# Kernel optimization log

Hardware: AMD Instinct MI355X
Metric: run time of the kernel (lower is better)

The kernel has to match this reference:

```python
import jax, jax.numpy as jnp
import numpy as np

BN_EPS = 1e-3  # Keras BatchNormalization default epsilon

def _conv2d_same(x, w, b):
    # x: NHWC, w: HWIO (kh,kw,2,1)
    y = jax.lax.conv_general_dilated(x, w, window_strides=(1, 1), padding='SAME',
                                     dimension_numbers=('NHWC', 'HWIO', 'NHWC'))
    return y + b

def _zpool(t):
    # concat([max, avg], axis=-1) over channel axis -> last dim = 2
    return jnp.concatenate([jnp.max(t, axis=-1, keepdims=True),
                            jnp.mean(t, axis=-1, keepdims=True)], axis=-1)

def _att_map(t2, w, b, g, beta, mean, var):
    y = _conv2d_same(t2, w, b)
    y = (y - mean) * jax.lax.rsqrt(var + BN_EPS) * g + beta  # inference BN
    return jax.nn.sigmoid(y)

def setup_inputs() -> dict:
    key = jax.random.key(0)
    ks = jax.random.split(key, 8)
    B, H, W, C, K, RR = 32, 56, 56, 256, 7, 8
    d = {}
    d['x'] = jax.random.normal(ks[0], (B, H, W, C), dtype=jnp.float32)
    for i, kk in zip((1, 2, 3), ks[1:4]):
        d[f'conv{i}_w'] = jax.random.normal(kk, (K, K, 2, 1), dtype=jnp.float32) * 0.1
        d[f'conv{i}_b'] = jnp.zeros((1,), dtype=jnp.float32)
        d[f'bn{i}_g'] = jnp.ones((1,), dtype=jnp.float32)
        d[f'bn{i}_b'] = jnp.zeros((1,), dtype=jnp.float32)
        d[f'bn{i}_m'] = jnp.zeros((1,), dtype=jnp.float32)
        d[f'bn{i}_v'] = jnp.ones((1,), dtype=jnp.float32)
    Ch = C // RR
    d['se_w1'] = jax.random.normal(ks[4], (C, Ch), dtype=jnp.float32) * (2.0 / C) ** 0.5
    d['se_b1'] = jnp.zeros((Ch,), dtype=jnp.float32)
    d['se_w2'] = jax.random.normal(ks[5], (Ch, C), dtype=jnp.float32) * 0.05
    d['se_b2'] = jnp.zeros((C,), dtype=jnp.float32)
    return d

def reference(x, conv1_w, conv1_b, bn1_g, bn1_b, bn1_m, bn1_v,
              conv2_w, conv2_b, bn2_g, bn2_b, bn2_m, bn2_v,
              conv3_w, conv3_b, bn3_g, bn3_b, bn3_m, bn3_v,
              se_w1, se_b1, se_w2, se_b2):
    # Branch 1 (H-axis): permute (B,H,W,C)->(B,H,C,W), pool over W
    th1 = jnp.transpose(x, (0, 1, 3, 2))
    a1 = _att_map(_zpool(th1), conv1_w, conv1_b, bn1_g, bn1_b, bn1_m, bn1_v)
    br1 = jnp.transpose(th1 * a1, (0, 1, 3, 2))
    # Branch 2 (W-axis): permute (B,H,W,C)->(B,C,W,H), pool over H
    th2 = jnp.transpose(x, (0, 3, 2, 1))
    a2 = _att_map(_zpool(th2), conv2_w, conv2_b, bn2_g, bn2_b, bn2_m, bn2_v)
    br2 = jnp.transpose(th2 * a2, (0, 3, 2, 1))
    # Branch 3 (identity): pool over C
    a3 = _att_map(_zpool(x), conv3_w, conv3_b, bn3_g, bn3_b, bn3_m, bn3_v)
    br3 = x * a3
    # TriSE1: Add branches, then SE channel gating
    s = br1 + br2 + br3
    gap = jnp.mean(s, axis=(1, 2), keepdims=True)            # (B,1,1,C)
    h = jax.nn.relu(jnp.einsum('bijc,cd->bijd', gap, se_w1) + se_b1)
    cw = jax.nn.sigmoid(jnp.einsum('bijd,dc->bijc', h, se_w2) + se_b2)
    return s * cw
```

## Files before the change

kernel.cpp:

```cpp
#include <hip/hip_runtime.h>
#include <math.h>

namespace {
constexpr int B = 32, H = 56, W = 56, C = 256;
constexpr int HW  = H * W;
constexpr int WC  = W * C;
constexpr int HC  = H * C;
constexpr int HWC = H * W * C;
constexpr int CH  = 32;
constexpr float BN_EPS = 1e-3f;

__device__ __forceinline__ float sigmoidf_(float v) { return 1.0f / (1.0f + expf(-v)); }
}

__global__ __launch_bounds__(256)
void pool_all_kernel(const float* __restrict__ x,
                     float* __restrict__ pmax1, float* __restrict__ pavg1,
                     float* __restrict__ pmax2, float* __restrict__ pavg2,
                     float* __restrict__ pmax3, float* __restrict__ pavg3) {
    const int t = threadIdx.x;
    const int lane = t & 63, sub = t >> 6;
    const int c4 = lane * 4;
    __shared__ float smx[4][256];
    __shared__ float ssm[4][256];

    if (blockIdx.x < B * H) {
        const int b = blockIdx.x / H, h = blockIdx.x % H;
        const float* xp = x + (size_t)b * HWC + (size_t)h * WC;
        float4 mx = make_float4(-INFINITY, -INFINITY, -INFINITY, -INFINITY);
        float4 sm = make_float4(0.f, 0.f, 0.f, 0.f);
        for (int wq = 0; wq < 14; ++wq) {
            const int w = wq * 4 + sub;
            const float4 v = *(const float4*)(xp + w * C + c4);
            mx.x = fmaxf(mx.x, v.x); mx.y = fmaxf(mx.y, v.y);
            mx.z = fmaxf(mx.z, v.z); mx.w = fmaxf(mx.w, v.w);
            sm.x += v.x; sm.y += v.y; sm.z += v.z; sm.w += v.w;
            float m3 = fmaxf(fmaxf(v.x, v.y), fmaxf(v.z, v.w));
            float s3 = v.x + v.y + v.z + v.w;
            #pragma unroll
            for (int off = 32; off > 0; off >>= 1) {
                m3 = fmaxf(m3, __shfl_down(m3, off));
                s3 += __shfl_down(s3, off);
            }
            if (lane == 0) {
                pmax3[b * HW + h * W + w] = m3;
                pavg3[b * HW + h * W + w] = s3 * (1.0f / C);
            }
        }
        *(float4*)&smx[sub][c4] = mx;
        *(float4*)&ssm[sub][c4] = sm;
        __syncthreads();
        const float m = fmaxf(fmaxf(smx[0][t], smx[1][t]), fmaxf(smx[2][t], smx[3][t]));
        const float s = ssm[0][t] + ssm[1][t] + ssm[2][t] + ssm[3][t];
        pmax1[b * HC + h * C + t] = m;
        pavg1[b * HC + h * C + t] = s * (1.0f / W);
    } else {
        const int tt = blockIdx.x - B * H;
        const int b = tt / W, w = tt % W;
        const float* xp = x + (size_t)b * HWC + (size_t)w * C;
        float4 mx = make_float4(-INFINITY, -INFINITY, -INFINITY, -INFINITY);
        float4 sm = make_float4(0.f, 0.f, 0.f, 0.f);
        for (int hq = 0; hq < 14; ++hq) {
            const int h = hq * 4 + sub;
            const float4 v = *(const float4*)(xp + (size_t)h * WC + c4);
            mx.x = fmaxf(mx.x, v.x); mx.y = fmaxf(mx.y, v.y);
            mx.z = fmaxf(mx.z, v.z); mx.w = fmaxf(mx.w, v.w);
            sm.x += v.x; sm.y += v.y; sm.z += v.z; sm.w += v.w;
        }
        *(float4*)&smx[sub][c4] = mx;
        *(float4*)&ssm[sub][c4] = sm;
        __syncthreads();
        const float m = fmaxf(fmaxf(smx[0][t], smx[1][t]), fmaxf(smx[2][t], smx[3][t]));
        const float s = ssm[0][t] + ssm[1][t] + ssm[2][t] + ssm[3][t];
        pmax2[b * WC + w * C + t] = m;
        pavg2[b * WC + w * C + t] = s * (1.0f / H);
    }
}

__global__ __launch_bounds__(256)
void conv_all_kernel(const float* __restrict__ pmax1, const float* __restrict__ pavg1,
                     const float* __restrict__ pmax2, const float* __restrict__ pavg2,
                     const float* __restrict__ pmax3, const float* __restrict__ pavg3,
                     const float* __restrict__ c1w, const float* __restrict__ c1b,
                     const float* __restrict__ g1,  const float* __restrict__ be1,
                     const float* __restrict__ m1,  const float* __restrict__ v1,
                     const float* __restrict__ c2w, const float* __restrict__ c2b,
                     const float* __restrict__ g2,  const float* __restrict__ be2,
                     const float* __restrict__ m2,  const float* __restrict__ v2,
                     const float* __restrict__ c3w, const float* __restrict__ c3b,
                     const float* __restrict__ g3,  const float* __restrict__ be3,
                     const float* __restrict__ m3,  const float* __restrict__ v3,
                     float* __restrict__ a1, float* __restrict__ a2t, float* __restrict__ a3) {
    const int t = threadIdx.x;
    __shared__ float wg[98];

    if (blockIdx.x < B * H) {
        if (t < 98) wg[t] = c1w[t];
        __syncthreads();
        const int b = blockIdx.x / H, h = blockIdx.x % H;
        const float A  = rsqrtf(v1[0] + BN_EPS) * g1[0];
        const float Bc = (c1b[0] - m1[0]) * A + be1[0];
        float acc = 0.f;
        const float* bm = pmax1 + b * HC;
        const float* ba = pavg1 + b * HC;
        #pragma unroll
        for (int ky = 0; ky < 7; ++ky) {
            const int hy = h + ky - 3;
            if (hy < 0 || hy >= H) continue;
            const float* rm = bm + hy * C;
            const float* ra = ba + hy * C;
            #pragma unroll
            for (int kx = 0; kx < 7; ++kx) {
                const int cx = t + kx - 3;
                if (cx < 0 || cx >= C) continue;
                acc += rm[cx] * wg[ky * 14 + kx * 2] + ra[cx] * wg[ky * 14 + kx * 2 + 1];
            }
        }
        a1[b * HC + h * C + t] = sigmoidf_(acc * A + Bc);
    } else if (blockIdx.x < 2 * B * H) {
        if (t < 98) wg[t] = c2w[t];
        __syncthreads();
        const int tt = blockIdx.x - B * H;
        const int b = tt / W, w = tt % W;
        const float A  = rsqrtf(v2[0] + BN_EPS) * g2[0];
        const float Bc = (c2b[0] - m2[0]) * A + be2[0];
        float acc = 0.f;
        #pragma unroll
        for (int kx = 0; kx < 7; ++kx) {
            const int wx = w + kx - 3;
            if (wx < 0 || wx >= W) continue;
            const float* rm = pmax2 + b * WC + wx * C;
            const float* ra = pavg2 + b * WC + wx * C;
            #pragma unroll
            for (int ky = 0; ky < 7; ++ky) {
                const int cy = t + ky - 3;
                if (cy < 0 || cy >= C) continue;
                acc += rm[cy] * wg[ky * 14 + kx * 2] + ra[cy] * wg[ky * 14 + kx * 2 + 1];
            }
        }
        a2t[b * WC + w * C + t] = sigmoidf_(acc * A + Bc);
    } else {
        if (t < 98) wg[t] = c3w[t];
        __syncthreads();
        const int gid = (blockIdx.x - 2 * B * H) * 256 + t;
        const int b = gid / HW;
        const int hw = gid % HW;
        const int h = hw / W, w = hw % W;
        const float A  = rsqrtf(v3[0] + BN_EPS) * g3[0];
        const float Bc = (c3b[0] - m3[0]) * A + be3[0];
        float acc = 0.f;
        const float* bm = pmax3 + b * HW;
        const float* ba = pavg3 + b * HW;
        #pragma unroll
        for (int ky = 0; ky < 7; ++ky) {
            const int hy = h + ky - 3;
            if (hy < 0 || hy >= H) continue;
            #pragma unroll
            for (int kx = 0; kx < 7; ++kx) {
                const int wx = w + kx - 3;
                if (wx < 0 || wx >= W) continue;
                acc += bm[hy * W + wx] * wg[ky * 14 + kx * 2] + ba[hy * W + wx] * wg[ky * 14 + kx * 2 + 1];
            }
        }
        a3[b * HW + hw] = sigmoidf_(acc * A + Bc);
    }
}

__global__ __launch_bounds__(256)
void gap_row_kernel(const float* __restrict__ x, const float* __restrict__ a1,
                    const float* __restrict__ a2t, const float* __restrict__ a3,
                    float* __restrict__ gpart) {
    const int b = blockIdx.x / H, h = blockIdx.x % H;
    const int t = threadIdx.x;
    const int lane = t & 63, sub = t >> 6;
    const int c4 = lane * 4;
    const float* xp  = x   + (size_t)b * HWC + (size_t)h * WC;
    const float* a2b = a2t + (size_t)b * WC;
    const float4 a1v = *(const float4*)(a1 + b * HC + h * C + c4);
    float4 acc = make_float4(0.f, 0.f, 0.f, 0.f);
    for (int wq = 0; wq < 14; ++wq) {
        const int w = wq * 4 + sub;
        const float4 xv  = *(const float4*)(xp  + w * C + c4);
        const float4 a2v = *(const float4*)(a2b + w * C + c4);
        const float a3v  = a3[b * HW + h * W + w];
        acc.x += xv.x * (a1v.x + a2v.x + a3v);
        acc.y += xv.y * (a1v.y + a2v.y + a3v);
        acc.z += xv.z * (a1v.z + a2v.z + a3v);
        acc.w += xv.w * (a1v.w + a2v.w + a3v);
    }
    __shared__ float sacc[4][256];
    *(float4*)&sacc[sub][c4] = acc;
    __syncthreads();
    gpart[(size_t)blockIdx.x * C + t] = sacc[0][t] + sacc[1][t] + sacc[2][t] + sacc[3][t];
}

__global__ __launch_bounds__(256)
void se_kernel(const float* __restrict__ gpart,
               const float* __restrict__ w1, const float* __restrict__ b1,
               const float* __restrict__ w2, const float* __restrict__ b2,
               float* __restrict__ cw) {
    const int b = blockIdx.x;
    const int t = threadIdx.x;
    __shared__ float gs[C];
    __shared__ float hs[CH];
    float s = 0.f;
    for (int r = 0; r < H; ++r) s += gpart[(size_t)(b * H + r) * C + t];
    gs[t] = s * (1.0f / (float)HW);
    __syncthreads();
    if (t < CH) {
        float a = b1[t];
        for (int c = 0; c < C; ++c) a += gs[c] * w1[c * CH + t];
        hs[t] = fmaxf(a, 0.f);
    }
    __syncthreads();
    float a = b2[t];
    #pragma unroll
    for (int d = 0; d < CH; ++d) a += hs[d] * w2[d * C + t];
    cw[b * C + t] = sigmoidf_(a);
}

__global__ __launch_bounds__(256)
void out_row_kernel(const float* __restrict__ x, const float* __restrict__ a1,
                    const float* __restrict__ a2t, const float* __restrict__ a3,
                    const float* __restrict__ cw, float* __restrict__ out) {
    const int b = blockIdx.x / H, h = blockIdx.x % H;
    const int t = threadIdx.x;
    const int lane = t & 63, sub = t >> 6;
    const int c4 = lane * 4;
    const float* xp  = x   + (size_t)b * HWC + (size_t)h * WC;
    const float* a2b = a2t + (size_t)b * WC;
    float*       op  = out + (size_t)b * HWC + (size_t)h * WC;
    const float4 a1v = *(const float4*)(a1 + b * HC + h * C + c4);
    const float4 cwv = *(const float4*)(cw + b * C + c4);
    for (int wq = 0; wq < 14; ++wq) {
        const int w = wq * 4 + sub;
        const float4 xv  = *(const float4*)(xp  + w * C + c4);
        const float4 a2v = *(const float4*)(a2b + w * C + c4);
        const float a3v  = a3[b * HW + h * W + w];
        float4 o;
        o.x = xv.x * (a1v.x + a2v.x + a3v) * cwv.x;
        o.y = xv.y * (a1v.y + a2v.y + a3v) * cwv.y;
        o.z = xv.z * (a1v.z + a2v.z + a3v) * cwv.z;
        o.w = xv.w * (a1v.w + a2v.w + a3v) * cwv.w;
        *(float4*)(op + w * C + c4) = o;
    }
}

extern "C" void kernel_launch(void* const* d_in, const int* in_sizes, int n_in,
                              void* d_out, int out_size, void* d_ws, size_t ws_size,
                              hipStream_t stream) {
    const float* x   = (const float*)d_in[0];
    const float* c1w = (const float*)d_in[1];  const float* c1b = (const float*)d_in[2];
    const float* g1  = (const float*)d_in[3];  const float* be1 = (const float*)d_in[4];
    const float* m1  = (const float*)d_in[5];  const float* v1  = (const float*)d_in[6];
    const float* c2w = (const float*)d_in[7];  const float* c2b = (const float*)d_in[8];
    const float* g2  = (const float*)d_in[9];  const float* be2 = (const float*)d_in[10];
    const float* m2  = (const float*)d_in[11]; const float* v2  = (const float*)d_in[12];
    const float* c3w = (const float*)d_in[13]; const float* c3b = (const float*)d_in[14];
    const float* g3  = (const float*)d_in[15]; const float* be3 = (const float*)d_in[16];
    const float* m3  = (const float*)d_in[17]; const float* v3  = (const float*)d_in[18];
    const float* sw1 = (const float*)d_in[19]; const float* sb1 = (const float*)d_in[20];
    const float* sw2 = (const float*)d_in[21]; const float* sb2 = (const float*)d_in[22];

    float* ws = (float*)d_ws;
    float* pmax1 = ws;
    float* pavg1 = pmax1 + (size_t)B * HC;
    float* pmax2 = pavg1 + (size_t)B * HC;
    float* pavg2 = pmax2 + (size_t)B * WC;
    float* pmax3 = pavg2 + (size_t)B * WC;
    float* pavg3 = pmax3 + (size_t)B * HW;
    float* a1    = pavg3 + (size_t)B * HW;
    float* a2t   = a1    + (size_t)B * HC;
    float* a3    = a2t   + (size_t)B * WC;
    float* gpart = a3    + (size_t)B * HW;
    float* cwv   = gpart + (size_t)B * H * C;

    pool_all_kernel<<<B * H + B * W, 256, 0, stream>>>(x, pmax1, pavg1, pmax2, pavg2, pmax3, pavg3);
    conv_all_kernel<<<2 * B * H + (B * HW) / 256, 256, 0, stream>>>(
        pmax1, pavg1, pmax2, pavg2, pmax3, pavg3,
        c1w, c1b, g1, be1, m1, v1,
        c2w, c2b, g2, be2, m2, v2,
        c3w, c3b, g3, be3, m3, v3,
        a1, a2t, a3);
    gap_row_kernel<<<B * H, 256, 0, stream>>>(x, a1, a2t, a3, gpart);
    se_kernel<<<B, 256, 0, stream>>>(gpart, sw1, sb1, sw2, sb2, cwv);
    out_row_kernel<<<B * H, 256, 0, stream>>>(x, a1, a2t, a3, cwv, (float*)d_out);
}
```

Measured before the change: 311.9 us.

## Factor GAP algebraically, stage conv inputs in LDS, restructure W-pool, nontemporal output

The global-average-pool sum for branches 1 and 2 is rewritten as a1·pavg1 and a2·pavg2 summed in the SE kernel, so gap_row only multiplies x by a3. That cuts the a1/a2 reads from the second full pass over x. The conv kernel stages the 7 needed pooled rows into zero-padded shared memory to drop the per-tap bounds checks. The W-axis pooling now gives each thread its own w column across all H rows, removing the LDS reduction and using far fewer blocks. Output stores become nontemporal. The fewer pooling blocks may reduce parallelism, and the SE kernel now does more serial work per batch.

```diff
diff --git a/kernel.cpp b/kernel.cpp
--- a/kernel.cpp
+++ b/kernel.cpp
@@ -10,7 +10,15 @@
 constexpr int CH  = 32;
 constexpr float BN_EPS = 1e-3f;
 
+using f4v = __attribute__((ext_vector_type(4))) float;
+
 __device__ __forceinline__ float sigmoidf_(float v) { return 1.0f / (1.0f + expf(-v)); }
+
+__device__ __forceinline__ void nt_store_float4(float* p, const float4& o) {
+    union { float4 s; f4v v; } u;
+    u.s = o;
+    __builtin_nontemporal_store(u.v, (f4v*)p);
+}
 }
 
 __global__ __launch_bounds__(256)
@@ -19,12 +27,12 @@
                      float* __restrict__ pmax2, float* __restrict__ pavg2,
                      float* __restrict__ pmax3, float* __restrict__ pavg3) {
     const int t = threadIdx.x;
-    const int lane = t & 63, sub = t >> 6;
-    const int c4 = lane * 4;
-    __shared__ float smx[4][256];
-    __shared__ float ssm[4][256];
 
     if (blockIdx.x < B * H) {
+        const int lane = t & 63, sub = t >> 6;
+        const int c4 = lane * 4;
+        __shared__ float smx[4][256];
+        __shared__ float ssm[4][256];
         const int b = blockIdx.x / H, h = blockIdx.x % H;
         const float* xp = x + (size_t)b * HWC + (size_t)h * WC;
         float4 mx = make_float4(-INFINITY, -INFINITY, -INFINITY, -INFINITY);
@@ -56,24 +64,25 @@
         pavg1[b * HC + h * C + t] = s * (1.0f / W);
     } else {
         const int tt = blockIdx.x - B * H;
-        const int b = tt / W, w = tt % W;
-        const float* xp = x + (size_t)b * HWC + (size_t)w * C;
+        const int b = tt / 14, wq = tt % 14;
+        const int w = wq * 4 + (t >> 6);
+        const int c4 = (t & 63) * 4;
+        const float* xp = x + (size_t)b * HWC + (size_t)w * C + c4;
         float4 mx = make_float4(-INFINITY, -INFINITY, -INFINITY, -INFINITY);
         float4 sm = make_float4(0.f, 0.f, 0.f, 0.f);
-        for (int hq = 0; hq < 14; ++hq) {
-            const int h = hq * 4 + sub;
-            const float4 v = *(const float4*)(xp + (size_t)h * WC + c4);
+        #pragma unroll 8
+        for (int h = 0; h < H; ++h) {
+            const float4 v = *(const float4*)(xp + (size_t)h * WC);
             mx.x = fmaxf(mx.x, v.x); mx.y = fmaxf(mx.y, v.y);
             mx.z = fmaxf(mx.z, v.z); mx.w = fmaxf(mx.w, v.w);
             sm.x += v.x; sm.y += v.y; sm.z += v.z; sm.w += v.w;
         }
-        *(float4*)&smx[sub][c4] = mx;
-        *(float4*)&ssm[sub][c4] = sm;
-        __syncthreads();
-        const float m = fmaxf(fmaxf(smx[0][t], smx[1][t]), fmaxf(smx[2][t], smx[3][t]));
-        const float s = ssm[0][t] + ssm[1][t] + ssm[2][t] + ssm[3][t];
-        pmax2[b * WC + w * C + t] = m;
-        pavg2[b * WC + w * C + t] = s * (1.0f / H);
+        const int oi = b * WC + w * C + c4;
+        *(float4*)(pmax2 + oi) = mx;
+        float4 av;
+        av.x = sm.x * (1.0f / H); av.y = sm.y * (1.0f / H);
+        av.z = sm.z * (1.0f / H); av.w = sm.w * (1.0f / H);
+        *(float4*)(pavg2 + oi) = av;
     }
 }
 
@@ -93,51 +102,59 @@
                      float* __restrict__ a1, float* __restrict__ a2t, float* __restrict__ a3) {
     const int t = threadIdx.x;
     __shared__ float wg[98];
+    __shared__ float sm[7][264];
+    __shared__ float sa[7][264];
 
     if (blockIdx.x < B * H) {
         if (t < 98) wg[t] = c1w[t];
+        const int b = blockIdx.x / H, h = blockIdx.x % H;
+        const float* bm = pmax1 + b * HC;
+        const float* ba = pavg1 + b * HC;
+        #pragma unroll
+        for (int ky = 0; ky < 7; ++ky) {
+            const int hy = h + ky - 3;
+            const bool val = (hy >= 0 && hy < H);
+            const int hyc = min(max(hy, 0), H - 1);
+            const float lm = bm[hyc * C + t];
+            const float la = ba[hyc * C + t];
+            sm[ky][t + 3] = val ? lm : 0.f;
+            sa[ky][t + 3] = val ? la : 0.f;
+            if (t < 3) { sm[ky][t] = 0.f; sa[ky][t] = 0.f; sm[ky][261 - t] = 0.f; sa[ky][261 - t] = 0.f; }
+        }
         __syncthreads();
-        const int b = blockIdx.x / H, h = blockIdx.x % H;
         const float A  = rsqrtf(v1[0] + BN_EPS) * g1[0];
         const float Bc = (c1b[0] - m1[0]) * A + be1[0];
         float acc = 0.f;
-        const float* bm = pmax1 + b * HC;
-        const float* ba = pavg1 + b * HC;
-        #pragma unroll
-        for (int ky = 0; ky < 7; ++ky) {
-            const int hy = h + ky - 3;
-            if (hy < 0 || hy >= H) continue;
-            const float* rm = bm + hy * C;
-            const float* ra = ba + hy * C;
+        #pragma unroll
+        for (int ky = 0; ky < 7; ++ky)
             #pragma unroll
-            for (int kx = 0; kx < 7; ++kx) {
-                const int cx = t + kx - 3;
-                if (cx < 0 || cx >= C) continue;
-                acc += rm[cx] * wg[ky * 14 + kx * 2] + ra[cx] * wg[ky * 14 + kx * 2 + 1];
-            }
-        }
+            for (int kx = 0; kx < 7; ++kx)
+                acc += sm[ky][t + kx] * wg[ky * 14 + kx * 2] + sa[ky][t + kx] * wg[ky * 14 + kx * 2 + 1];
         a1[b * HC + h * C + t] = sigmoidf_(acc * A + Bc);
     } else if (blockIdx.x < 2 * B * H) {
         if (t < 98) wg[t] = c2w[t];
-        __syncthreads();
         const int tt = blockIdx.x - B * H;
         const int b = tt / W, w = tt % W;
+        #pragma unroll
+        for (int kx = 0; kx < 7; ++kx) {
+            const int wx = w + kx - 3;
+            const bool val = (wx >= 0 && wx < W);
+            const int wxc = min(max(wx, 0), W - 1);
+            const float lm = pmax2[b * WC + wxc * C + t];
+            const float la = pavg2[b * WC + wxc * C + t];
+            sm[kx][t + 3] = val ? lm : 0.f;
+            sa[kx][t + 3] = val ? la : 0.f;
+            if (t < 3) { sm[kx][t] = 0.f; sa[kx][t] = 0.f; sm[kx][261 - t] = 0.f; sa[kx][261 - t] = 0.f; }
+        }
+        __syncthreads();
         const float A  = rsqrtf(v2[0] + BN_EPS) * g2[0];
         const float Bc = (c2b[0] - m2[0]) * A + be2[0];
         float acc = 0.f;
         #pragma unroll
-        for (int kx = 0; kx < 7; ++kx) {
-            const int wx = w + kx - 3;
-            if (wx < 0 || wx >= W) continue;
-            const float* rm = pmax2 + b * WC + wx * C;
-            const float* ra = pavg2 + b * WC + wx * C;
+        for (int kx = 0; kx < 7; ++kx)
             #pragma unroll
-            for (int ky = 0; ky < 7; ++ky) {
-                const int cy = t + ky - 3;
-                if (cy < 0 || cy >= C) continue;
-                acc += rm[cy] * wg[ky * 14 + kx * 2] + ra[cy] * wg[ky * 14 + kx * 2 + 1];
-            }
-        }
+            for (int ky = 0; ky < 7; ++ky)
+                acc += sm[kx][t + ky] * wg[ky * 14 + kx * 2] + sa[kx][t + ky] * wg[ky * 14 + kx * 2 + 1];
         a2t[b * WC + w * C + t] = sigmoidf_(acc * A + Bc);
     } else {
         if (t < 98) wg[t] = c3w[t];
@@ -167,26 +184,22 @@
 }
 
 __global__ __launch_bounds__(256)
-void gap_row_kernel(const float* __restrict__ x, const float* __restrict__ a1,
-                    const float* __restrict__ a2t, const float* __restrict__ a3,
+void gap_row_kernel(const float* __restrict__ x, const float* __restrict__ a3,
                     float* __restrict__ gpart) {
     const int b = blockIdx.x / H, h = blockIdx.x % H;
     const int t = threadIdx.x;
     const int lane = t & 63, sub = t >> 6;
     const int c4 = lane * 4;
-    const float* xp  = x   + (size_t)b * HWC + (size_t)h * WC;
-    const float* a2b = a2t + (size_t)b * WC;
-    const float4 a1v = *(const float4*)(a1 + b * HC + h * C + c4);
+    const float* xp = x + (size_t)b * HWC + (size_t)h * WC;
     float4 acc = make_float4(0.f, 0.f, 0.f, 0.f);
     for (int wq = 0; wq < 14; ++wq) {
         const int w = wq * 4 + sub;
-        const float4 xv  = *(const float4*)(xp  + w * C + c4);
-        const float4 a2v = *(const float4*)(a2b + w * C + c4);
-        const float a3v  = a3[b * HW + h * W + w];
-        acc.x += xv.x * (a1v.x + a2v.x + a3v);
-        acc.y += xv.y * (a1v.y + a2v.y + a3v);
-        acc.z += xv.z * (a1v.z + a2v.z + a3v);
-        acc.w += xv.w * (a1v.w + a2v.w + a3v);
+        const float4 xv = *(const float4*)(xp + w * C + c4);
+        const float a3v = a3[b * HW + h * W + w];
+        acc.x += xv.x * a3v;
+        acc.y += xv.y * a3v;
+        acc.z += xv.z * a3v;
+        acc.w += xv.w * a3v;
     }
     __shared__ float sacc[4][256];
     *(float4*)&sacc[sub][c4] = acc;
@@ -196,6 +209,8 @@
 
 __global__ __launch_bounds__(256)
 void se_kernel(const float* __restrict__ gpart,
+               const float* __restrict__ a1,  const float* __restrict__ pavg1,
+               const float* __restrict__ a2t, const float* __restrict__ pavg2,
                const float* __restrict__ w1, const float* __restrict__ b1,
                const float* __restrict__ w2, const float* __restrict__ b2,
                float* __restrict__ cw) {
@@ -203,9 +218,13 @@
     const int t = threadIdx.x;
     __shared__ float gs[C];
     __shared__ float hs[CH];
-    float s = 0.f;
-    for (int r = 0; r < H; ++r) s += gpart[(size_t)(b * H + r) * C + t];
-    gs[t] = s * (1.0f / (float)HW);
+    float s1 = 0.f, s2 = 0.f, s3 = 0.f;
+    for (int r = 0; r < H; ++r) {
+        s1 += a1 [b * HC + r * C + t] * pavg1[b * HC + r * C + t];
+        s2 += a2t[b * WC + r * C + t] * pavg2[b * WC + r * C + t];
+        s3 += gpart[(size_t)(b * H + r) * C + t];
+    }
+    gs[t] = (s1 + s2) * (1.0f / 56.0f) + s3 * (1.0f / (float)HW);
     __syncthreads();
     if (t < CH) {
         float a = b1[t];
@@ -242,7 +261,7 @@
         o.y = xv.y * (a1v.y + a2v.y + a3v) * cwv.y;
         o.z = xv.z * (a1v.z + a2v.z + a3v) * cwv.z;
         o.w = xv.w * (a1v.w + a2v.w + a3v) * cwv.w;
-        *(float4*)(op + w * C + c4) = o;
+        nt_store_float4(op + w * C + c4, o);
     }
 }
 
@@ -275,14 +294,14 @@
     float* gpart = a3    + (size_t)B * HW;
     float* cwv   = gpart + (size_t)B * H * C;
 
-    pool_all_kernel<<<B * H + B * W, 256, 0, stream>>>(x, pmax1, pavg1, pmax2, pavg2, pmax3, pavg3);
+    pool_all_kernel<<<B * H + B * 14, 256, 0, stream>>>(x, pmax1, pavg1, pmax2, pavg2, pmax3, pavg3);
     conv_all_kernel<<<2 * B * H + (B * HW) / 256, 256, 0, stream>>>(
         pmax1, pavg1, pmax2, pavg2, pmax3, pavg3,
         c1w, c1b, g1, be1, m1, v1,
         c2w, c2b, g2, be2, m2, v2,
         c3w, c3b, g3, be3, m3, v3,
         a1, a2t, a3);
-    gap_row_kernel<<<B * H, 256, 0, stream>>>(x, a1, a2t, a3, gpart);
-    se_kernel<<<B, 256, 0, stream>>>(gpart, sw1, sb1, sw2, sb2, cwv);
+    gap_row_kernel<<<B * H, 256, 0, stream>>>(x, a3, gpart);
+    se_kernel<<<B, 256, 0, stream>>>(gpart, a1, pavg1, a2t, pavg2, sw1, sb1, sw2, sb2, cwv);
     out_row_kernel<<<B * H, 256, 0, stream>>>(x, a1, a2t, a3, cwv, (float*)d_out);
 }
```

After: 295.8 us. -5.2%, faster.
